# Kernel optimization log

Hardware: AMD Instinct MI355X
Metric: run time of the kernel (lower is better)

The kernel has to match this reference:

```python
import jax, jax.numpy as jnp
import numpy as np

DECAY = 0.8  # voltage decay (init arg)

# ThresholdActivation: spike = (v > 0), straight-through surrogate gradient
@jax.custom_vjp
def spike(x):
    return (x > 0).astype(x.dtype)

def _spike_fwd(x):
    return (x > 0).astype(x.dtype), None

def _spike_bwd(res, g):
    return (g,)

spike.defvjp(_spike_fwd, _spike_bwd)


def setup_inputs() -> dict:
    key = jax.random.key(0)
    k1, k2, k3 = jax.random.split(key, 3)
    B, I, H, T = 128, 512, 512, 512
    x = jax.random.normal(k1, (B, I, T), dtype=jnp.float32)
    # torch: nn.init.normal_(w, 0.1, 0.1)
    W = 0.1 + 0.1 * jax.random.normal(k2, (I, H), dtype=jnp.float32)
    b = 0.1 + 0.1 * jax.random.normal(k3, (1, H), dtype=jnp.float32)
    return {"x": x, "W": W, "b": b}


def reference(x, W, b):
    # x: (B, I, T), W: (I, H), b: (1, H)
    B, I, T = x.shape
    H = W.shape[1]
    xt = jnp.transpose(x, (2, 0, 1))              # (T, B, I)
    xw = jnp.einsum('tbi,ih->tbh', xt, W)         # batch all input matmuls: (T, B, H)

    def step(carry, xw_t):
        h, y = carry
        # s_t = relu(Wx + decay * s_{t-1} * (1 - y_{t-1}))
        h = jax.nn.relu(xw_t + DECAY * h * (1.0 - y))
        # y_t = threshold(s_t + bias)
        y = spike(h + b)
        return (h, y), y

    init = (jnp.zeros((B, H), x.dtype), jnp.zeros((B, H), x.dtype))
    _, ys = jax.lax.scan(step, init, xw)          # ys: (T, B, H)
    outputs = jnp.transpose(ys, (1, 2, 0))        # (B, H, T)
    # SNU applies SpikeActivation to the concatenated outputs
    return spike(outputs)
```

## Files before the change

kernel.cpp:

```cpp
#include <hip/hip_runtime.h>


#define DECAYF 0.8f
#define PART   ((size_t)512 * 128 * 128)
#define PARTF4 (PART / 4)

__device__ __forceinline__ int block_compact(const float* __restrict__ bias,
                                             int* idx_s, int* cnt_s) {
    const int tid = threadIdx.x;
    if (tid < 64) {
        int base = 0;
        #pragma unroll
        for (int w = 0; w < 8; w++) {
            bool p = bias[w * 64 + tid] <= 0.0f;
            unsigned long long m = __ballot(p);
            if (p) idx_s[base + __popcll(m & ((1ull << tid) - 1ull))] = w * 64 + tid;
            base += __popcll(m);
        }
        if (tid == 0) cnt_s[0] = base;
    }
    __syncthreads();
    const int total = cnt_s[0];
    const int i0 = (total > 0) ? idx_s[0] : 0;
    for (int j = total + tid; j < 256; j += blockDim.x) idx_s[j] = i0;
    __syncthreads();
    return total;
}

__global__ __launch_bounds__(256) void gather_W(const float* __restrict__ bias,
                                                const float* __restrict__ W,
                                                float* __restrict__ Wc) {
    __shared__ int idx_s[256];
    __shared__ int cnt_s[1];
    block_compact(bias, idx_s, cnt_s);
    const int i = blockIdx.x;
    const int j = threadIdx.x;
    Wc[i * 256 + j] = W[i * 512 + idx_s[j]];
}

__global__ __launch_bounds__(256) void gemm_split(const float* __restrict__ x,
                                                  const float* __restrict__ Wc,
                                                  const float* __restrict__ bias,
                                                  float* __restrict__ xwp,
                                                  float* __restrict__ xwc1) {
    const int kc = blockIdx.x;
    const int tid = threadIdx.x;
    int kbeg, kend, coff;
    float* op;
    if (kc < 4) { kbeg = kc * 128; kend = kbeg + 128; coff = 0;   op = xwp + (size_t)kc * PART; }
    else {
        __shared__ int cnt_s;
        if (tid < 64) {
            int tot = 0;
            #pragma unroll
            for (int w = 0; w < 8; w++)
                tot += __popcll(__ballot(bias[w * 64 + tid] <= 0.0f));
            if (tid == 0) cnt_s = tot;
        }
        __syncthreads();
        if (cnt_s <= 128) return;
        kbeg = 0; kend = 512; coff = 128; op = xwc1;
    }
    const int I = 512, T = 512, NC = 256;
    const int b  = blockIdx.z;
    const int t0 = blockIdx.y * 128;

    __shared__ float As[16][132];
    __shared__ float Bs[16][132];

    const int wave = tid >> 6;
    const int lane = tid & 63;
    const int lx = lane & 7;
    const int ly = lane >> 3;
    const int m_base = ((wave >> 1) << 6) + ly * 8;
    const int n_base = ((wave & 1) << 6) + lx * 8;

    float acc[8][8];
    #pragma unroll
    for (int i = 0; i < 8; i++)
        #pragma unroll
        for (int j = 0; j < 8; j++) acc[i][j] = 0.f;

    const float* xb = x + (size_t)b * I * T;

    for (int k0 = kbeg; k0 < kend; k0 += 16) {
        #pragma unroll
        for (int j = 0; j < 2; j++) {
            int id2 = tid + j * 256;
            int row = id2 >> 5;
            int c4  = (id2 & 31) << 2;
            *(float4*)&As[row][c4] = *(const float4*)(xb + (size_t)(k0 + row) * T + t0 + c4);
            *(float4*)&Bs[row][c4] = *(const float4*)(Wc + (size_t)(k0 + row) * NC + coff + c4);
        }
        __syncthreads();
        #pragma unroll
        for (int kk = 0; kk < 16; kk++) {
            float a[8], bb[8];
            *(float4*)&a[0]  = *(const float4*)&As[kk][m_base];
            *(float4*)&a[4]  = *(const float4*)&As[kk][m_base + 4];
            *(float4*)&bb[0] = *(const float4*)&Bs[kk][n_base];
            *(float4*)&bb[4] = *(const float4*)&Bs[kk][n_base + 4];
            #pragma unroll
            for (int mi = 0; mi < 8; mi++)
                #pragma unroll
                for (int ni = 0; ni < 8; ni++)
                    acc[mi][ni] = fmaf(a[mi], bb[ni], acc[mi][ni]);
        }
        __syncthreads();
    }

    #pragma unroll
    for (int mi = 0; mi < 8; mi++) {
        int t = t0 + m_base + mi;
        float* o = op + ((size_t)t * 128 + b) * 128 + n_base;
        *(float4*)o       = *(float4*)&acc[mi][0];
        *(float4*)(o + 4) = *(float4*)&acc[mi][4];
    }
}

__global__ __launch_bounds__(512) void scan_fill(const float* __restrict__ xwp,
                                                 const float* __restrict__ xwc1,
                                                 const float* __restrict__ bias,
                                                 float* __restrict__ out) {
    const int T = 512;
    const int id  = blockIdx.x;
    const int tid = threadIdx.x;

    if (id >= 512 && id < 1536) {
        const float4 ones = make_float4(1.f, 1.f, 1.f, 1.f);
        float4* out4 = (float4*)out;
        const size_t base = (size_t)(id - 512) * 8192 + tid;
        #pragma unroll
        for (int q = 0; q < 16; q++) {
            size_t f4 = base + (size_t)q * 512;
            int h = (int)((f4 >> 7) & 511);
            if (bias[h] > 0.0f) out4[f4] = ones;
        }
        return;
    }

    __shared__ int idx_s[256];
    __shared__ int cnt_s[1];
    __shared__ float4 win[2][16][4][8];
    const int count = block_compact(bias, idx_s, cnt_s);

    if (id >= 1536) {
        if (count <= 128) return;
        if (tid >= count - 128) return;
        const int b = id - 1536;
        const int j = 128 + tid;
        const int h = idx_s[j];
        const float bv = bias[h];
        const float* p = xwc1 + (size_t)b * 128 + tid;
        float* o = out + ((size_t)b * 512 + h) * (size_t)T;
        const size_t STR = (size_t)128 * 128;
        float hs = 0.f, y = 0.f;
        float nx[8];
        #pragma unroll
        for (int d = 0; d < 8; d++) nx[d] = p[(size_t)d * STR];
        for (int t0 = 0; t0 < T; t0 += 8) {
            float cur[8], yb[8];
            #pragma unroll
            for (int d = 0; d < 8; d++) cur[d] = nx[d];
            const bool more = (t0 + 8) < T;
            #pragma unroll
            for (int d = 0; d < 8; d++)
                nx[d] = more ? p[(size_t)(t0 + 8 + d) * STR] : 0.f;
            #pragma unroll
            for (int d = 0; d < 8; d++) {
                hs = fmaf(DECAYF * hs, 1.f - y, cur[d]);
                hs = fmaxf(hs, 0.f);
                y  = (hs + bv > 0.f) ? 1.f : 0.f;
                yb[d] = y;
            }
            *(float4*)(o + t0)     = *(float4*)&yb[0];
            *(float4*)(o + t0 + 4) = *(float4*)&yb[4];
        }
        return;
    }

    const int b  = id >> 2;
    const int jq = id & 3;
    if (jq * 32 >= count) return;

    const float4* xwp4 = (const float4*)xwp;
    const int j4l  = tid & 7;
    const int pp   = (tid >> 3) & 3;
    const int toff = tid >> 5;
    const size_t src_base = (size_t)pp * PARTF4 + (size_t)b * 32 + jq * 8 + j4l;

    const int jl = tid;
    const int j  = jq * 32 + jl;
    const bool active = (tid < 32) && (j < count);
    const int h = active ? idx_s[j] : 0;
    const float bv = active ? bias[h] : 0.f;
    float* o = out + ((size_t)b * 512 + h) * (size_t)T;
    float hs = 0.f, y = 0.f;

    const float* winf = (const float*)win;

    {
        float4 v = xwp4[src_base + (size_t)toff * 128 * 32];
        win[0][toff][pp][j4l] = v;
    }
    __syncthreads();

    for (int w = 0; w < 32; w++) {
        const int buf = w & 1;
        float4 v;
        const bool more = (w + 1) < 32;
        if (more)
            v = xwp4[src_base + (size_t)((w + 1) * 16 + toff) * 128 * 32];

        if (active) {
            float yb[16];
            #pragma unroll
            for (int d = 0; d < 16; d++) {
                const int rb = ((buf * 16 + d) * 4) * 32 + jl;
                float s = (winf[rb] + winf[rb + 32]) + (winf[rb + 64] + winf[rb + 96]);
                hs = fmaf(DECAYF * hs, 1.f - y, s);
                hs = fmaxf(hs, 0.f);
                y  = (hs + bv > 0.f) ? 1.f : 0.f;
                yb[d] = y;
            }
            const int t0 = w * 16;
            *(float4*)(o + t0)      = *(float4*)&yb[0];
            *(float4*)(o + t0 + 4)  = *(float4*)&yb[4];
            *(float4*)(o + t0 + 8)  = *(float4*)&yb[8];
            *(float4*)(o + t0 + 12) = *(float4*)&yb[12];
        }
        if (more)
            win[buf ^ 1][toff][pp][j4l] = v;
        __syncthreads();
    }
}

extern "C" void kernel_launch(void* const* d_in, const int* in_sizes, int n_in,
                              void* d_out, int out_size, void* d_ws, size_t ws_size,
                              hipStream_t stream) {
    const float* x    = (const float*)d_in[0];
    const float* W    = (const float*)d_in[1];
    const float* bias = (const float*)d_in[2];
    float* out = (float*)d_out;

    char* ws = (char*)d_ws;
    float* Wc   = (float*)(ws + 4096);
    float* xwp  = (float*)(ws + ((size_t)1 << 20));
    float* xwc1 = (float*)(ws + ((size_t)129 << 20));

    gather_W<<<512, 256, 0, stream>>>(bias, W, Wc);
    dim3 g1(5, 4, 128);
    gemm_split<<<g1, 256, 0, stream>>>(x, Wc, bias, xwp, xwc1);
    scan_fill<<<1664, 512, 0, stream>>>(xwp, xwc1, bias, out);
}
```

Measured before the change: 344.6 us.

## Double-buffer GEMM shared tiles and restructure scan into 64-thread register-prefetch blocks

The GEMM now uses double-buffered shared-memory tiles, issuing global loads for the next k-slice into registers while it computes on the current one, so each iteration needs one barrier instead of two. The scan kernel is reorganised into 64-thread blocks in which every thread reads its four partial sums straight from global memory with a 16-deep register prefetch, replacing the shared-memory window and its per-step block barriers. The fill and overflow sections are re-gridded to match. This removes barrier stalls and idle lanes (the old scan kept only 32 of 512 threads active), at the cost of more registers and uncoalesced-looking strided scalar loads.

```diff
diff --git a/kernel.cpp b/kernel.cpp
--- a/kernel.cpp
+++ b/kernel.cpp
@@ -3,7 +3,6 @@
 
 #define DECAYF 0.8f
 #define PART   ((size_t)512 * 128 * 128)
-#define PARTF4 (PART / 4)
 
 __device__ __forceinline__ int block_compact(const float* __restrict__ bias,
                                              int* idx_s, int* cnt_s) {
@@ -65,8 +64,8 @@
     const int b  = blockIdx.z;
     const int t0 = blockIdx.y * 128;
 
-    __shared__ float As[16][132];
-    __shared__ float Bs[16][132];
+    __shared__ float As[2][16][132];
+    __shared__ float Bs[2][16][132];
 
     const int wave = tid >> 6;
     const int lane = tid & 63;
@@ -83,29 +82,45 @@
 
     const float* xb = x + (size_t)b * I * T;
 
-    for (int k0 = kbeg; k0 < kend; k0 += 16) {
-        #pragma unroll
-        for (int j = 0; j < 2; j++) {
-            int id2 = tid + j * 256;
-            int row = id2 >> 5;
-            int c4  = (id2 & 31) << 2;
-            *(float4*)&As[row][c4] = *(const float4*)(xb + (size_t)(k0 + row) * T + t0 + c4);
-            *(float4*)&Bs[row][c4] = *(const float4*)(Wc + (size_t)(k0 + row) * NC + coff + c4);
-        }
-        __syncthreads();
+    const int r0 = tid >> 5;
+    const int c0 = (tid & 31) << 2;
+    float4 ra0, ra1, rb0, rb1;
+
+    auto LOAD = [&](int k0) {
+        ra0 = *(const float4*)(xb + (size_t)(k0 + r0    ) * T + t0 + c0);
+        ra1 = *(const float4*)(xb + (size_t)(k0 + r0 + 8) * T + t0 + c0);
+        rb0 = *(const float4*)(Wc + (size_t)(k0 + r0    ) * NC + coff + c0);
+        rb1 = *(const float4*)(Wc + (size_t)(k0 + r0 + 8) * NC + coff + c0);
+    };
+    auto STORE = [&](int bf) {
+        *(float4*)&As[bf][r0    ][c0] = ra0;
+        *(float4*)&As[bf][r0 + 8][c0] = ra1;
+        *(float4*)&Bs[bf][r0    ][c0] = rb0;
+        *(float4*)&Bs[bf][r0 + 8][c0] = rb1;
+    };
+
+    LOAD(kbeg);
+    STORE(0);
+    __syncthreads();
+
+    int buf = 0;
+    for (int k0 = kbeg; k0 < kend; k0 += 16, buf ^= 1) {
+        const bool more = (k0 + 16) < kend;
+        if (more) LOAD(k0 + 16);
         #pragma unroll
         for (int kk = 0; kk < 16; kk++) {
             float a[8], bb[8];
-            *(float4*)&a[0]  = *(const float4*)&As[kk][m_base];
-            *(float4*)&a[4]  = *(const float4*)&As[kk][m_base + 4];
-            *(float4*)&bb[0] = *(const float4*)&Bs[kk][n_base];
-            *(float4*)&bb[4] = *(const float4*)&Bs[kk][n_base + 4];
+            *(float4*)&a[0]  = *(const float4*)&As[buf][kk][m_base];
+            *(float4*)&a[4]  = *(const float4*)&As[buf][kk][m_base + 4];
+            *(float4*)&bb[0] = *(const float4*)&Bs[buf][kk][n_base];
+            *(float4*)&bb[4] = *(const float4*)&Bs[buf][kk][n_base + 4];
             #pragma unroll
             for (int mi = 0; mi < 8; mi++)
                 #pragma unroll
                 for (int ni = 0; ni < 8; ni++)
                     acc[mi][ni] = fmaf(a[mi], bb[ni], acc[mi][ni]);
         }
+        if (more) STORE(buf ^ 1);
         __syncthreads();
     }
 
@@ -118,21 +133,23 @@
     }
 }
 
-__global__ __launch_bounds__(512) void scan_fill(const float* __restrict__ xwp,
-                                                 const float* __restrict__ xwc1,
-                                                 const float* __restrict__ bias,
-                                                 float* __restrict__ out) {
+__global__ __launch_bounds__(64) void scan_fill(const float* __restrict__ xwp,
+                                                const float* __restrict__ xwc1,
+                                                const float* __restrict__ bias,
+                                                float* __restrict__ out) {
     const int T = 512;
+    const size_t TS = (size_t)128 * 128;
     const int id  = blockIdx.x;
     const int tid = threadIdx.x;
 
-    if (id >= 512 && id < 1536) {
+    if (id >= 256 && id < 4352) {
+        const int fid = id - 256;
         const float4 ones = make_float4(1.f, 1.f, 1.f, 1.f);
         float4* out4 = (float4*)out;
-        const size_t base = (size_t)(id - 512) * 8192 + tid;
-        #pragma unroll
-        for (int q = 0; q < 16; q++) {
-            size_t f4 = base + (size_t)q * 512;
+        const size_t base = (size_t)fid * 2048 + tid;
+        #pragma unroll
+        for (int q = 0; q < 32; q++) {
+            size_t f4 = base + (size_t)q * 64;
             int h = (int)((f4 >> 7) & 511);
             if (bias[h] > 0.0f) out4[f4] = ones;
         }
@@ -141,97 +158,82 @@
 
     __shared__ int idx_s[256];
     __shared__ int cnt_s[1];
-    __shared__ float4 win[2][16][4][8];
     const int count = block_compact(bias, idx_s, cnt_s);
 
-    if (id >= 1536) {
+    if (id >= 4352) {
         if (count <= 128) return;
-        if (tid >= count - 128) return;
-        const int b = id - 1536;
-        const int j = 128 + tid;
+        const int oid = id - 4352;
+        const int b  = oid >> 1;
+        const int j  = 128 + (oid & 1) * 64 + tid;
+        if (j >= count) return;
         const int h = idx_s[j];
         const float bv = bias[h];
-        const float* p = xwc1 + (size_t)b * 128 + tid;
+        const float* p = xwc1 + (size_t)b * 128 + (j - 128);
         float* o = out + ((size_t)b * 512 + h) * (size_t)T;
-        const size_t STR = (size_t)128 * 128;
         float hs = 0.f, y = 0.f;
-        float nx[8];
-        #pragma unroll
-        for (int d = 0; d < 8; d++) nx[d] = p[(size_t)d * STR];
-        for (int t0 = 0; t0 < T; t0 += 8) {
-            float cur[8], yb[8];
-            #pragma unroll
-            for (int d = 0; d < 8; d++) cur[d] = nx[d];
-            const bool more = (t0 + 8) < T;
-            #pragma unroll
-            for (int d = 0; d < 8; d++)
-                nx[d] = more ? p[(size_t)(t0 + 8 + d) * STR] : 0.f;
-            #pragma unroll
-            for (int d = 0; d < 8; d++) {
-                hs = fmaf(DECAYF * hs, 1.f - y, cur[d]);
-                hs = fmaxf(hs, 0.f);
-                y  = (hs + bv > 0.f) ? 1.f : 0.f;
-                yb[d] = y;
-            }
-            *(float4*)(o + t0)     = *(float4*)&yb[0];
-            *(float4*)(o + t0 + 4) = *(float4*)&yb[4];
-        }
-        return;
-    }
-
-    const int b  = id >> 2;
-    const int jq = id & 3;
-    if (jq * 32 >= count) return;
-
-    const float4* xwp4 = (const float4*)xwp;
-    const int j4l  = tid & 7;
-    const int pp   = (tid >> 3) & 3;
-    const int toff = tid >> 5;
-    const size_t src_base = (size_t)pp * PARTF4 + (size_t)b * 32 + jq * 8 + j4l;
-
-    const int jl = tid;
-    const int j  = jq * 32 + jl;
-    const bool active = (tid < 32) && (j < count);
-    const int h = active ? idx_s[j] : 0;
-    const float bv = active ? bias[h] : 0.f;
-    float* o = out + ((size_t)b * 512 + h) * (size_t)T;
-    float hs = 0.f, y = 0.f;
-
-    const float* winf = (const float*)win;
-
-    {
-        float4 v = xwp4[src_base + (size_t)toff * 128 * 32];
-        win[0][toff][pp][j4l] = v;
-    }
-    __syncthreads();
-
-    for (int w = 0; w < 32; w++) {
-        const int buf = w & 1;
-        float4 v;
-        const bool more = (w + 1) < 32;
-        if (more)
-            v = xwp4[src_base + (size_t)((w + 1) * 16 + toff) * 128 * 32];
-
-        if (active) {
+        float nx[16];
+        #pragma unroll
+        for (int d = 0; d < 16; d++) nx[d] = p[(size_t)d * TS];
+        for (int t0 = 0; t0 < T; t0 += 16) {
+            const bool more = (t0 + 16) < T;
             float yb[16];
             #pragma unroll
             for (int d = 0; d < 16; d++) {
-                const int rb = ((buf * 16 + d) * 4) * 32 + jl;
-                float s = (winf[rb] + winf[rb + 32]) + (winf[rb + 64] + winf[rb + 96]);
+                float s = nx[d];
+                if (more) nx[d] = p[(size_t)(t0 + 16 + d) * TS];
                 hs = fmaf(DECAYF * hs, 1.f - y, s);
                 hs = fmaxf(hs, 0.f);
                 y  = (hs + bv > 0.f) ? 1.f : 0.f;
                 yb[d] = y;
             }
-            const int t0 = w * 16;
             *(float4*)(o + t0)      = *(float4*)&yb[0];
             *(float4*)(o + t0 + 4)  = *(float4*)&yb[4];
             *(float4*)(o + t0 + 8)  = *(float4*)&yb[8];
             *(float4*)(o + t0 + 12) = *(float4*)&yb[12];
         }
-        if (more)
-            win[buf ^ 1][toff][pp][j4l] = v;
-        __syncthreads();
+        return;
+    }
+
+    const int b  = id >> 1;
+    const int j  = (id & 1) * 64 + tid;
+    if (j >= count) return;
+    const int h = idx_s[j];
+    const float bv = bias[h];
+    const float* p0 = xwp + (size_t)b * 128 + j;
+    float* o = out + ((size_t)b * 512 + h) * (size_t)T;
+
+    float hs = 0.f, y = 0.f;
+    float nx0[16], nx1[16], nx2[16], nx3[16];
+    #pragma unroll
+    for (int d = 0; d < 16; d++) {
+        size_t a = (size_t)d * TS;
+        nx0[d] = p0[a];
+        nx1[d] = p0[PART + a];
+        nx2[d] = p0[2 * PART + a];
+        nx3[d] = p0[3 * PART + a];
+    }
+    for (int t0 = 0; t0 < T; t0 += 16) {
+        const bool more = (t0 + 16) < T;
+        float yb[16];
+        #pragma unroll
+        for (int d = 0; d < 16; d++) {
+            float s = (nx0[d] + nx1[d]) + (nx2[d] + nx3[d]);
+            if (more) {
+                size_t a = (size_t)(t0 + 16 + d) * TS;
+                nx0[d] = p0[a];
+                nx1[d] = p0[PART + a];
+                nx2[d] = p0[2 * PART + a];
+                nx3[d] = p0[3 * PART + a];
+            }
+            hs = fmaf(DECAYF * hs, 1.f - y, s);
+            hs = fmaxf(hs, 0.f);
+            y  = (hs + bv > 0.f) ? 1.f : 0.f;
+            yb[d] = y;
+        }
+        *(float4*)(o + t0)      = *(float4*)&yb[0];
+        *(float4*)(o + t0 + 4)  = *(float4*)&yb[4];
+        *(float4*)(o + t0 + 8)  = *(float4*)&yb[8];
+        *(float4*)(o + t0 + 12) = *(float4*)&yb[12];
     }
 }
 
@@ -251,5 +253,5 @@
     gather_W<<<512, 256, 0, stream>>>(bias, W, Wc);
     dim3 g1(5, 4, 128);
     gemm_split<<<g1, 256, 0, stream>>>(x, Wc, bias, xwp, xwc1);
-    scan_fill<<<1664, 512, 0, stream>>>(xwp, xwc1, bias, out);
-}
+    scan_fill<<<4608, 64, 0, stream>>>(xwp, xwc1, bias, out);
+}
```

Result: slower. 652.8 us (+89.5%).

## Double-buffer GEMM tiles with direct global-to-LDS async loads

Applied to the files above, without the earlier changes.

Replaces the register-staged tile loads in the input-projection GEMM with global_load_lds 16-byte direct-to-LDS transfers. It also adds a second LDS buffer so the next K-tile is prefetched while the current one is computed. This aims to hide global memory latency and save VGPRs and instructions on the load path. It drops the row padding (132 to 128) and relies on the single end-of-iteration barrier to order the async loads, which risks bank conflicts and synchronisation hazards.

```diff
diff --git a/kernel.cpp b/kernel.cpp
--- a/kernel.cpp
+++ b/kernel.cpp
@@ -65,8 +65,8 @@
     const int b  = blockIdx.z;
     const int t0 = blockIdx.y * 128;
 
-    __shared__ float As[16][132];
-    __shared__ float Bs[16][132];
+    __shared__ float As[2][16][128];
+    __shared__ float Bs[2][16][128];
 
     const int wave = tid >> 6;
     const int lane = tid & 63;
@@ -83,23 +83,35 @@
 
     const float* xb = x + (size_t)b * I * T;
 
-    for (int k0 = kbeg; k0 < kend; k0 += 16) {
-        #pragma unroll
-        for (int j = 0; j < 2; j++) {
-            int id2 = tid + j * 256;
-            int row = id2 >> 5;
-            int c4  = (id2 & 31) << 2;
-            *(float4*)&As[row][c4] = *(const float4*)(xb + (size_t)(k0 + row) * T + t0 + c4);
-            *(float4*)&Bs[row][c4] = *(const float4*)(Wc + (size_t)(k0 + row) * NC + coff + c4);
-        }
-        __syncthreads();
+    const int r0 = tid >> 5;
+    const int c0 = (tid & 31) << 2;
+
+    #define GLD16(gp, lp) \
+        __builtin_amdgcn_global_load_lds( \
+            (const __attribute__((address_space(1))) void*)(gp), \
+            (__attribute__((address_space(3))) void*)(lp), 16, 0, 0)
+
+    auto STAGE = [&](int k0, int bf) {
+        GLD16(xb + (size_t)(k0 + r0    ) * T + t0   + c0, &As[bf][r0    ][c0]);
+        GLD16(xb + (size_t)(k0 + r0 + 8) * T + t0   + c0, &As[bf][r0 + 8][c0]);
+        GLD16(Wc + (size_t)(k0 + r0    ) * NC + coff + c0, &Bs[bf][r0    ][c0]);
+        GLD16(Wc + (size_t)(k0 + r0 + 8) * NC + coff + c0, &Bs[bf][r0 + 8][c0]);
+    };
+
+    STAGE(kbeg, 0);
+    __syncthreads();
+
+    int buf = 0;
+    for (int k0 = kbeg; k0 < kend; k0 += 16, buf ^= 1) {
+        const bool more = (k0 + 16) < kend;
+        if (more) STAGE(k0 + 16, buf ^ 1);
         #pragma unroll
         for (int kk = 0; kk < 16; kk++) {
             float a[8], bb[8];
-            *(float4*)&a[0]  = *(const float4*)&As[kk][m_base];
-            *(float4*)&a[4]  = *(const float4*)&As[kk][m_base + 4];
-            *(float4*)&bb[0] = *(const float4*)&Bs[kk][n_base];
-            *(float4*)&bb[4] = *(const float4*)&Bs[kk][n_base + 4];
+            *(float4*)&a[0]  = *(const float4*)&As[buf][kk][m_base];
+            *(float4*)&a[4]  = *(const float4*)&As[buf][kk][m_base + 4];
+            *(float4*)&bb[0] = *(const float4*)&Bs[buf][kk][n_base];
+            *(float4*)&bb[4] = *(const float4*)&Bs[buf][kk][n_base + 4];
             #pragma unroll
             for (int mi = 0; mi < 8; mi++)
                 #pragma unroll
@@ -108,6 +120,7 @@
         }
         __syncthreads();
     }
+    #undef GLD16
 
     #pragma unroll
     for (int mi = 0; mi < 8; mi++) {
```

New measurement: 373.4 us. 1.08x slower.

## Drop split-K partials in GEMM and read single accumulated xw in scan

Applied to the files above, without the earlier changes.

The GEMM stops splitting K into four partial outputs that the scan kernel summed; each block now runs the full K=512 loop and writes a single xw buffer. The scan kernel loads one value per timestep instead of four, with a larger 64-step shared window. This removes 3/4 of the intermediate write and read traffic, but cuts GEMM grid parallelism from 4 to 1 K-slices per tile, which may leave the GPU underoccupied.

```diff
diff --git a/kernel.cpp b/kernel.cpp
--- a/kernel.cpp
+++ b/kernel.cpp
@@ -2,8 +2,6 @@
 
 
 #define DECAYF 0.8f
-#define PART   ((size_t)512 * 128 * 128)
-#define PARTF4 (PART / 4)
 
 __device__ __forceinline__ int block_compact(const float* __restrict__ bias,
                                              int* idx_s, int* cnt_s) {
@@ -41,13 +39,13 @@
 __global__ __launch_bounds__(256) void gemm_split(const float* __restrict__ x,
                                                   const float* __restrict__ Wc,
                                                   const float* __restrict__ bias,
-                                                  float* __restrict__ xwp,
+                                                  float* __restrict__ xw,
                                                   float* __restrict__ xwc1) {
     const int kc = blockIdx.x;
     const int tid = threadIdx.x;
-    int kbeg, kend, coff;
+    int coff;
     float* op;
-    if (kc < 4) { kbeg = kc * 128; kend = kbeg + 128; coff = 0;   op = xwp + (size_t)kc * PART; }
+    if (kc == 0) { coff = 0; op = xw; }
     else {
         __shared__ int cnt_s;
         if (tid < 64) {
@@ -59,7 +57,7 @@
         }
         __syncthreads();
         if (cnt_s <= 128) return;
-        kbeg = 0; kend = 512; coff = 128; op = xwc1;
+        coff = 128; op = xwc1;
     }
     const int I = 512, T = 512, NC = 256;
     const int b  = blockIdx.z;
@@ -83,7 +81,7 @@
 
     const float* xb = x + (size_t)b * I * T;
 
-    for (int k0 = kbeg; k0 < kend; k0 += 16) {
+    for (int k0 = 0; k0 < 512; k0 += 16) {
         #pragma unroll
         for (int j = 0; j < 2; j++) {
             int id2 = tid + j * 256;
@@ -118,7 +116,7 @@
     }
 }
 
-__global__ __launch_bounds__(512) void scan_fill(const float* __restrict__ xwp,
+__global__ __launch_bounds__(512) void scan_fill(const float* __restrict__ xw,
                                                  const float* __restrict__ xwc1,
                                                  const float* __restrict__ bias,
                                                  float* __restrict__ out) {
@@ -141,7 +139,6 @@
 
     __shared__ int idx_s[256];
     __shared__ int cnt_s[1];
-    __shared__ float4 win[2][16][4][8];
     const int count = block_compact(bias, idx_s, cnt_s);
 
     if (id >= 1536) {
@@ -183,11 +180,13 @@
     const int jq = id & 3;
     if (jq * 32 >= count) return;
 
-    const float4* xwp4 = (const float4*)xwp;
+    const float4* xw4 = (const float4*)xw;
     const int j4l  = tid & 7;
-    const int pp   = (tid >> 3) & 3;
-    const int toff = tid >> 5;
-    const size_t src_base = (size_t)pp * PARTF4 + (size_t)b * 32 + jq * 8 + j4l;
+    const int toff = tid >> 3;
+    const size_t src_base = (size_t)b * 32 + jq * 8 + j4l;
+
+    __shared__ float4 win4[2][512];
+    const float* winf = (const float*)win4;
 
     const int jl = tid;
     const int j  = jq * 32 + jl;
@@ -197,40 +196,38 @@
     float* o = out + ((size_t)b * 512 + h) * (size_t)T;
     float hs = 0.f, y = 0.f;
 
-    const float* winf = (const float*)win;
-
-    {
-        float4 v = xwp4[src_base + (size_t)toff * 128 * 32];
-        win[0][toff][pp][j4l] = v;
-    }
+    win4[0][tid] = xw4[(size_t)toff * 4096 + src_base];
     __syncthreads();
 
-    for (int w = 0; w < 32; w++) {
+    for (int w = 0; w < 8; w++) {
         const int buf = w & 1;
         float4 v;
-        const bool more = (w + 1) < 32;
+        const bool more = (w + 1) < 8;
         if (more)
-            v = xwp4[src_base + (size_t)((w + 1) * 16 + toff) * 128 * 32];
+            v = xw4[(size_t)((w + 1) * 64 + toff) * 4096 + src_base];
 
         if (active) {
-            float yb[16];
-            #pragma unroll
-            for (int d = 0; d < 16; d++) {
-                const int rb = ((buf * 16 + d) * 4) * 32 + jl;
-                float s = (winf[rb] + winf[rb + 32]) + (winf[rb + 64] + winf[rb + 96]);
-                hs = fmaf(DECAYF * hs, 1.f - y, s);
-                hs = fmaxf(hs, 0.f);
-                y  = (hs + bv > 0.f) ? 1.f : 0.f;
-                yb[d] = y;
+            const int t0w = w * 64;
+            #pragma unroll
+            for (int s = 0; s < 4; s++) {
+                float yb[16];
+                #pragma unroll
+                for (int d = 0; d < 16; d++) {
+                    float sv = winf[(size_t)(buf * 512 + (s * 16 + d) * 8) * 4 + jl];
+                    hs = fmaf(DECAYF * hs, 1.f - y, sv);
+                    hs = fmaxf(hs, 0.f);
+                    y  = (hs + bv > 0.f) ? 1.f : 0.f;
+                    yb[d] = y;
+                }
+                const int t0 = t0w + s * 16;
+                *(float4*)(o + t0)      = *(float4*)&yb[0];
+                *(float4*)(o + t0 + 4)  = *(float4*)&yb[4];
+                *(float4*)(o + t0 + 8)  = *(float4*)&yb[8];
+                *(float4*)(o + t0 + 12) = *(float4*)&yb[12];
             }
-            const int t0 = w * 16;
-            *(float4*)(o + t0)      = *(float4*)&yb[0];
-            *(float4*)(o + t0 + 4)  = *(float4*)&yb[4];
-            *(float4*)(o + t0 + 8)  = *(float4*)&yb[8];
-            *(float4*)(o + t0 + 12) = *(float4*)&yb[12];
         }
         if (more)
-            win[buf ^ 1][toff][pp][j4l] = v;
+            win4[buf ^ 1][tid] = v;
         __syncthreads();
     }
 }
@@ -245,11 +242,11 @@
 
     char* ws = (char*)d_ws;
     float* Wc   = (float*)(ws + 4096);
-    float* xwp  = (float*)(ws + ((size_t)1 << 20));
-    float* xwc1 = (float*)(ws + ((size_t)129 << 20));
+    float* xw   = (float*)(ws + ((size_t)1 << 20));
+    float* xwc1 = (float*)(ws + ((size_t)40 << 20));
 
     gather_W<<<512, 256, 0, stream>>>(bias, W, Wc);
-    dim3 g1(5, 4, 128);
-    gemm_split<<<g1, 256, 0, stream>>>(x, Wc, bias, xwp, xwc1);
-    scan_fill<<<1664, 512, 0, stream>>>(xwp, xwc1, bias, out);
-}
+    dim3 g1(2, 4, 128);
+    gemm_split<<<g1, 256, 0, stream>>>(x, Wc, bias, xw, xwc1);
+    scan_fill<<<1664, 512, 0, stream>>>(xw, xwc1, bias, out);
+}
```

After: 387.8 us. +12.5%, slower.
